# Performance work log

Hardware: AMD Instinct MI355X
Metric: run time of the kernel (lower is better)

Reference implementation:

```python
import jax, jax.numpy as jnp
from jax import lax
import numpy as np

B, H, W, D_MODEL = 2, 64, 64, 192
D_INNER, D_STATE, DT_RANK = 384, 16, 12
L = H * W
LN_EPS = 1e-5


def setup_inputs() -> dict:
    ks = jax.random.split(jax.random.key(0), 12)
    rng = np.random.default_rng(0)
    perm = rng.permutation(L).astype(np.int32)

    def p(i, shape, scale=0.02):
        return jax.random.normal(ks[i], shape, dtype=jnp.float32) * scale

    return {
        "x": jax.random.normal(ks[0], (B, H, W, D_MODEL), dtype=jnp.float32),
        "condition": jax.random.normal(ks[1], (B, H, W, D_MODEL), dtype=jnp.float32),
        "W_in": p(2, (2 * D_INNER, D_MODEL)),
        "W_con": p(3, (D_INNER, D_MODEL)),
        "conv_w": p(4, (D_INNER, 1, 3, 3)),
        "conv_b": jnp.zeros((D_INNER,), jnp.float32),
        "con_conv_w": p(5, (D_INNER, 1, 3, 3)),
        "con_conv_b": jnp.zeros((D_INNER,), jnp.float32),
        "x_proj_w": p(6, (DT_RANK + 2 * D_STATE, D_INNER)),
        "dt_proj_w": p(7, (D_INNER, DT_RANK)),
        "dt_proj_b": p(8, (D_INNER,), 0.1),
        "A_logs": jnp.tile(jnp.log(jnp.arange(1, D_STATE + 1, dtype=jnp.float32))[None, :], (D_INNER, 1)),
        "Ds": jnp.ones((D_INNER,), jnp.float32),
        "ln_w": jnp.ones((D_INNER,), jnp.float32),
        "ln_b": jnp.zeros((D_INNER,), jnp.float32),
        "W_out": p(9, (D_MODEL, D_INNER)),
        "scan_path": jnp.asarray(perm),
        "rev_scan_path": jnp.asarray(np.argsort(perm).astype(np.int32)),
    }


def _dwconv(x, w, b):
    # depthwise 3x3 conv, SAME padding; x: [B, C, H, W], w: [C, 1, 3, 3]
    y = lax.conv_general_dilated(x, w, (1, 1), "SAME",
                                 dimension_numbers=("NCHW", "OIHW", "NCHW"),
                                 feature_group_count=x.shape[1])
    return y + b[None, :, None, None]


def _selective_scan(u, delta, A, Bs, Cs, D):
    # u, delta: [B, D, L]; A: [D, N]; Bs, Cs: [B, N, L]; D: [D]
    dA = jnp.exp(jnp.einsum("bdl,dn->lbdn", delta, A))          # [L, B, D, N]
    dBu = jnp.einsum("bdl,bnl,bdl->lbdn", delta, Bs, u)          # [L, B, D, N]
    Ct = jnp.transpose(Cs, (2, 0, 1))                             # [L, B, N]
    h0 = jnp.zeros(dA.shape[1:], dA.dtype)

    def step(h, inp):
        a, b, c = inp
        h = a * h + b
        return h, jnp.einsum("bdn,bn->bd", h, c)

    _, ys = lax.scan(step, h0, (dA, dBu, Ct))                     # ys: [L, B, D]
    y = jnp.transpose(ys, (1, 2, 0))                              # [B, D, L]
    return y + u * D[None, :, None]


def _forward(x, condition, W_in, W_con, conv_w, conv_b, con_conv_w, con_conv_b,
             x_proj_w, dt_proj_w, dt_proj_b, A_logs, Ds, ln_w, ln_b, W_out,
             scan_path, rev_scan_path):
    b, h, w, _ = x.shape
    l = h * w
    xz = x @ W_in.T                                               # [B, H, W, 2*Din]
    xa, z = jnp.split(xz, 2, axis=-1)
    z = jax.nn.silu(z)
    c = condition @ W_con.T
    xa = jax.nn.silu(_dwconv(jnp.transpose(xa, (0, 3, 1, 2)), conv_w, conv_b))
    c = jax.nn.silu(_dwconv(jnp.transpose(c, (0, 3, 1, 2)), con_conv_w, con_conv_b))
    d = xa.shape[1]
    xs = xa.reshape(b, d, l)[:, :, scan_path]                     # forward_permutation, K=1
    cs = c.reshape(b, d, l)[:, :, scan_path]
    x_dbl = jnp.einsum("bdl,cd->bcl", xs + cs, x_proj_w)          # [B, R+2N, L]
    r, n = dt_proj_w.shape[1], A_logs.shape[1]
    dts = jnp.einsum("brl,dr->bdl", x_dbl[:, :r], dt_proj_w)
    Bs = x_dbl[:, r:r + n]
    Cs = x_dbl[:, r + n:]
    A = -jnp.exp(A_logs)
    delta = jax.nn.softplus(dts + dt_proj_b[None, :, None])       # delta_softplus=True
    y = _selective_scan(xs, delta, A, Bs, Cs, Ds)                 # [B, D, L]
    y = y[:, :, rev_scan_path]                                    # backward_permutation
    y = jnp.transpose(y, (0, 2, 1))                               # [B, L, D]
    mu = jnp.mean(y, axis=-1, keepdims=True)
    var = jnp.var(y, axis=-1, keepdims=True)
    y = (y - mu) * lax.rsqrt(var + LN_EPS) * ln_w + ln_b          # out_norm
    y = y.reshape(b, h, w, d) * z
    return y @ W_out.T                                            # out_proj (no bias)


def reference(x, condition, W_in, W_con, conv_w, conv_b, con_conv_w, con_conv_b,
              x_proj_w, dt_proj_w, dt_proj_b, A_logs, Ds, ln_w, ln_b, W_out,
              scan_path, rev_scan_path):
    return _forward(x, condition, W_in, W_con, conv_w, conv_b, con_conv_w,
                    con_conv_b, x_proj_w, dt_proj_w, dt_proj_b, A_logs, Ds,
                    ln_w, ln_b, W_out, scan_path, rev_scan_path)
```

## Files before the change

kernel.cpp:

```cpp
#include <hip/hip_runtime.h>
#include <math.h>

#define BB 2
#define HH 64
#define WW 64
#define DM 192
#define DI 384
#define NS 16
#define DTR 12
#define LL 4096
#define ROWS (BB*LL)
#define NCHUNK 128
#define LCHUNK 32
#define NCOMB 448
#define CSTRIDE ((size_t)BB * DI * 8)

typedef __attribute__((ext_vector_type(8))) short bf16x8;
typedef __attribute__((ext_vector_type(4))) float f32x4;

typedef __attribute__((address_space(3))) void        as3_void;
typedef __attribute__((address_space(1))) const void  as1_cvoid;

__device__ __forceinline__ void gl_lds16(const unsigned short* g, unsigned short* l) {
    __builtin_amdgcn_global_load_lds((as1_cvoid*)g, (as3_void*)l, 16, 0, 0);
}

#define WAITCNT_BARRIER(N)                                         \
    do {                                                           \
        asm volatile("s_waitcnt vmcnt(" #N ")" ::: "memory");      \
        __builtin_amdgcn_s_barrier();                              \
        asm volatile("" ::: "memory");                             \
    } while (0)

__device__ __forceinline__ float silu_f(float v) {
    return v / (1.0f + __expf(-v));
}

__device__ __forceinline__ unsigned short f2bf(float f) {
    union { float f; unsigned int u; } c; c.f = f;
    unsigned int u = c.u;
    u += 0x7fffu + ((u >> 16) & 1u);
    return (unsigned short)(u >> 16);
}
__device__ __forceinline__ float bf2f(unsigned short h) {
    union { unsigned int u; float f; } c; c.u = ((unsigned int)h) << 16;
    return c.f;
}

__global__ __launch_bounds__(256) void prep_weights(
    const float* __restrict__ x, const float* __restrict__ cond,
    const float* __restrict__ w_in, const float* __restrict__ w_con,
    const float* __restrict__ w_out,
    const float* __restrict__ x_proj_w, const float* __restrict__ dt_w,
    unsigned short* __restrict__ w_in_bf, unsigned short* __restrict__ w_con_bf,
    unsigned short* __restrict__ w_out_bf, unsigned short* __restrict__ wc,
    unsigned short* __restrict__ x_bfo, unsigned short* __restrict__ c_bfo)
{
    int idx = blockIdx.x * 256 + threadIdx.x;
    if (idx < 73728) {
        const float4* src; ushort4* dst; int off;
        if (idx < 36864)      { src = (const float4*)w_in;  dst = (ushort4*)w_in_bf;  off = idx; }
        else if (idx < 55296) { src = (const float4*)w_con; dst = (ushort4*)w_con_bf; off = idx - 36864; }
        else                  { src = (const float4*)w_out; dst = (ushort4*)w_out_bf; off = idx - 55296; }
        float4 v = src[off];
        ushort4 o;
        o.x = f2bf(v.x); o.y = f2bf(v.y); o.z = f2bf(v.z); o.w = f2bf(v.w);
        dst[off] = o;
    } else if (idx < 73728 + NCOMB * DI) {
        int e = idx - 73728;
        int row = e / DI, k = e - row * DI;
        float v = 0.f;
        if (row < 384) {
            const float* dw = dt_w + row * DTR;
            #pragma unroll
            for (int r = 0; r < DTR; ++r) v += dw[r] * x_proj_w[r * DI + k];
        } else if (row < 416) {
            v = x_proj_w[(12 + (row - 384)) * DI + k];
        }
        wc[e] = f2bf(v);
    } else if (idx < 73728 + NCOMB * DI + 786432) {
        int e = idx - (73728 + NCOMB * DI);
        const float4* src; ushort4* dst; int off;
        if (e < 393216) { src = (const float4*)x;    dst = (ushort4*)x_bfo; off = e; }
        else            { src = (const float4*)cond; dst = (ushort4*)c_bfo; off = e - 393216; }
        float4 v = src[off];
        ushort4 o;
        o.x = f2bf(v.x); o.y = f2bf(v.y); o.z = f2bf(v.z); o.w = f2bf(v.w);
        dst[off] = o;
    }
}

__global__ __launch_bounds__(256) void gemm_in(
    const unsigned short* __restrict__ x_bf, const unsigned short* __restrict__ cin_bf,
    const unsigned short* __restrict__ w_in_bf,
    const unsigned short* __restrict__ w_con_bf,
    unsigned short* __restrict__ xa_bf, unsigned short* __restrict__ z_bf,
    unsigned short* __restrict__ c_bf)
{
    const int y  = blockIdx.y;
    const int zz = (y >= 12) ? 1 : 0;
    const unsigned short* A = zz ? cin_bf : x_bf;
    const unsigned short* W = zz ? w_con_bf : w_in_bf;
    const int bn = (zz ? (y - 12) : y) * 64;
    const int bm = blockIdx.x * 64;

    __shared__ __align__(16) unsigned short sA[4 * 64 * 32];
    __shared__ __align__(16) unsigned short sB[4 * 64 * 32];
    const int tid  = threadIdx.x;
    const int wave = tid >> 6;
    const int lane = tid & 63;
    const int quad = lane >> 4;
    const int l16  = lane & 15;
    const int srow = tid >> 2;
    const int scol = ((tid & 3) ^ ((tid >> 3) & 3)) * 8;
    const int rswz = (quad ^ ((l16 >> 1) & 3)) * 8;

    f32x4 acc[4];
    #pragma unroll
    for (int t = 0; t < 4; ++t) acc[t] = (f32x4)(0.f);

    const unsigned short* gA = &A[(size_t)(bm + srow) * DM + scol];
    const unsigned short* gB = &W[(size_t)(bn + srow) * DM + scol];

    #pragma unroll
    for (int p = 0; p < 3; ++p) {
        gl_lds16(gA + p * 32, &sA[p * 2048 + wave * 512]);
        gl_lds16(gB + p * 32, &sB[p * 2048 + wave * 512]);
    }
    WAITCNT_BARRIER(4);

    const int ar = (wave * 16 + l16) * 32 + rswz;

    #pragma unroll
    for (int t = 0; t < 6; ++t) {
        if (t + 3 < 6) {
            const int k = (t + 3) * 32, pb = (t + 3) & 3;
            gl_lds16(gA + k, &sA[pb * 2048 + wave * 512]);
            gl_lds16(gB + k, &sB[pb * 2048 + wave * 512]);
        }
        const unsigned short* cA = &sA[(t & 3) * 2048];
        const unsigned short* cB = &sB[(t & 3) * 2048];
        bf16x8 a = *(bf16x8*)&cA[ar];
        #pragma unroll
        for (int n = 0; n < 4; ++n) {
            bf16x8 b = *(bf16x8*)&cB[(n * 16 + l16) * 32 + rswz];
            acc[n] = __builtin_amdgcn_mfma_f32_16x16x32_bf16(a, b, acc[n], 0, 0, 0);
        }
        if (t < 5) {
            if (t + 3 < 6)      WAITCNT_BARRIER(4);
            else if (t + 2 < 6) WAITCNT_BARRIER(2);
            else                WAITCNT_BARRIER(0);
        }
    }

    #pragma unroll
    for (int n = 0; n < 4; ++n) {
        int col = bn + n * 16 + l16;
        #pragma unroll
        for (int r = 0; r < 4; ++r) {
            int row = bm + wave * 16 + quad * 4 + r;
            float v = acc[n][r];
            if (zz == 0) {
                if (col < 384) xa_bf[(size_t)row * 384 + col] = f2bf(v);
                else           z_bf[(size_t)row * 384 + (col - 384)] = f2bf(silu_f(v));
            } else {
                c_bf[(size_t)row * 384 + col] = f2bf(v);
            }
        }
    }
}

__global__ __launch_bounds__(256) void gemm_comb(
    const unsigned short* __restrict__ A, const unsigned short* __restrict__ W,
    const float* __restrict__ bias, float* __restrict__ btct,
    unsigned short* __restrict__ du_lo)
{
    __shared__ __align__(16) unsigned short sA[4 * 64 * 32];
    __shared__ __align__(16) unsigned short sB[4 * 64 * 32];
    const int bm = blockIdx.x * 64;
    const int bn = blockIdx.y * 64;
    const int tid  = threadIdx.x;
    const int wave = tid >> 6;
    const int lane = tid & 63;
    const int quad = lane >> 4;
    const int l16  = lane & 15;
    const int srow = tid >> 2;
    const int scol = ((tid & 3) ^ ((tid >> 3) & 3)) * 8;
    const int rswz = (quad ^ ((l16 >> 1) & 3)) * 8;

    f32x4 acc[4];
    #pragma unroll
    for (int t = 0; t < 4; ++t) acc[t] = (f32x4)(0.f);

    const unsigned short* gA = &A[(size_t)(bm + srow) * DI + scol];
    const unsigned short* gB = &W[(size_t)(bn + srow) * DI + scol];

    #pragma unroll
    for (int p = 0; p < 3; ++p) {
        gl_lds16(gA + p * 32, &sA[p * 2048 + wave * 512]);
        gl_lds16(gB + p * 32, &sB[p * 2048 + wave * 512]);
    }
    WAITCNT_BARRIER(4);

    const int ar = (wave * 16 + l16) * 32 + rswz;

    #pragma unroll
    for (int t = 0; t < 12; ++t) {
        if (t + 3 < 12) {
            const int k = (t + 3) * 32, pb = (t + 3) & 3;
            gl_lds16(gA + k, &sA[pb * 2048 + wave * 512]);
            gl_lds16(gB + k, &sB[pb * 2048 + wave * 512]);
        }
        const unsigned short* cA = &sA[(t & 3) * 2048];
        const unsigned short* cB = &sB[(t & 3) * 2048];
        bf16x8 a = *(bf16x8*)&cA[ar];
        #pragma unroll
        for (int n = 0; n < 4; ++n) {
            bf16x8 b = *(bf16x8*)&cB[(n * 16 + l16) * 32 + rswz];
            acc[n] = __builtin_amdgcn_mfma_f32_16x16x32_bf16(a, b, acc[n], 0, 0, 0);
        }
        if (t < 11) {
            if (t + 3 < 12)      WAITCNT_BARRIER(4);
            else if (t + 2 < 12) WAITCNT_BARRIER(2);
            else                 WAITCNT_BARRIER(0);
        }
    }

    #pragma unroll
    for (int n = 0; n < 4; ++n) {
        int col = bn + n * 16 + l16;
        #pragma unroll
        for (int r = 0; r < 4; ++r) {
            int row = bm + wave * 16 + quad * 4 + r;
            float v = acc[n][r];
            if (col < 384) {
                float a = v + bias[col];
                float sp = (a > 20.f) ? a : log1pf(__expf(a));
                du_lo[((size_t)row * 384 + col) * 2] = f2bf(sp);
            } else if (col < 416) {
                int idx = col - 384;
                int pos = (idx < 16) ? ((idx & 7) * 4 + (idx >> 3))
                                     : (((idx - 16) & 7) * 4 + 2 + ((idx - 16) >> 3));
                btct[(size_t)row * 32 + pos] = v;
            }
        }
    }
}

__global__ __launch_bounds__(256) void gemm_out_fused(
    const unsigned short* __restrict__ yt, const unsigned short* __restrict__ z,
    const int* __restrict__ rev_path,
    const float* __restrict__ ln_w, const float* __restrict__ ln_b,
    const unsigned short* __restrict__ W, float* __restrict__ out)
{
    __shared__ __align__(16) unsigned short sA[32 * 392];
    __shared__ __align__(16) unsigned short sB[3 * 64 * 32];
    const int bm = blockIdx.x * 32;
    const int bn = blockIdx.y * 64;
    const int tid = threadIdx.x;
    const int r2  = tid >> 3;
    const int q8  = tid & 7;
    const int b   = bm >> 12;
    const int l   = (bm & (LL - 1)) + r2;
    const int js  = rev_path[l];

    const unsigned short* yrow = yt + ((size_t)(b * LL + js)) * DI;
    const unsigned short* zrow = z  + ((size_t)(b * LL + l)) * DI;

    bf16x8 yv[6];
    float s = 0.f, s2 = 0.f;
    #pragma unroll
    for (int i = 0; i < 6; ++i) {
        yv[i] = *(const bf16x8*)&yrow[i * 64 + q8 * 8];
        #pragma unroll
        for (int e = 0; e < 8; ++e) {
            float f = bf2f((unsigned short)yv[i][e]);
            s += f; s2 += f * f;
        }
    }
    s  += __shfl_xor(s, 1);  s  += __shfl_xor(s, 2);  s  += __shfl_xor(s, 4);
    s2 += __shfl_xor(s2, 1); s2 += __shfl_xor(s2, 2); s2 += __shfl_xor(s2, 4);
    const float mu  = s * (1.0f / DI);
    const float inv = rsqrtf(s2 * (1.0f / DI) - mu * mu + 1e-5f);

    #pragma unroll
    for (int i = 0; i < 6; ++i) {
        int c = i * 64 + q8 * 8;
        bf16x8 zv = *(const bf16x8*)&zrow[c];
        float4 wa = *(const float4*)&ln_w[c];
        float4 wb = *(const float4*)&ln_w[c + 4];
        float4 ba = *(const float4*)&ln_b[c];
        float4 bb = *(const float4*)&ln_b[c + 4];
        bf16x8 o;
        o[0] = (short)f2bf(((bf2f((unsigned short)yv[i][0]) - mu) * inv * wa.x + ba.x) * bf2f((unsigned short)zv[0]));
        o[1] = (short)f2bf(((bf2f((unsigned short)yv[i][1]) - mu) * inv * wa.y + ba.y) * bf2f((unsigned short)zv[1]));
        o[2] = (short)f2bf(((bf2f((unsigned short)yv[i][2]) - mu) * inv * wa.z + ba.z) * bf2f((unsigned short)zv[2]));
        o[3] = (short)f2bf(((bf2f((unsigned short)yv[i][3]) - mu) * inv * wa.w + ba.w) * bf2f((unsigned short)zv[3]));
        o[4] = (short)f2bf(((bf2f((unsigned short)yv[i][4]) - mu) * inv * wb.x + bb.x) * bf2f((unsigned short)zv[4]));
        o[5] = (short)f2bf(((bf2f((unsigned short)yv[i][5]) - mu) * inv * wb.y + bb.y) * bf2f((unsigned short)zv[5]));
        o[6] = (short)f2bf(((bf2f((unsigned short)yv[i][6]) - mu) * inv * wb.z + bb.z) * bf2f((unsigned short)zv[6]));
        o[7] = (short)f2bf(((bf2f((unsigned short)yv[i][7]) - mu) * inv * wb.w + bb.w) * bf2f((unsigned short)zv[7]));
        *(bf16x8*)&sA[r2 * 392 + c] = o;
    }

    const int wave = tid >> 6;
    const int lane = tid & 63;
    const int quad = lane >> 4;
    const int l16  = lane & 15;
    const int srow = tid >> 2;
    const int scol = ((tid & 3) ^ ((tid >> 3) & 3)) * 8;
    const int rswz = (quad ^ ((l16 >> 1) & 3)) * 8;
    const int rf   = wave >> 1;
    const int np   = (wave & 1) * 2;

    f32x4 acc[2];
    acc[0] = (f32x4)(0.f); acc[1] = (f32x4)(0.f);

    const unsigned short* gB = &W[(size_t)(bn + srow) * DI + scol];
    const int abase = (rf * 16 + l16) * 392 + quad * 8;

    gl_lds16(gB,      &sB[0 * 2048 + wave * 512]);
    gl_lds16(gB + 32, &sB[1 * 2048 + wave * 512]);
    __syncthreads();

    #pragma unroll
    for (int t = 0; t < 12; ++t) {
        if (t + 2 < 12)
            gl_lds16(gB + (t + 2) * 32, &sB[((t + 2) % 3) * 2048 + wave * 512]);
        bf16x8 a = *(bf16x8*)&sA[abase + t * 32];
        const unsigned short* cB = &sB[(t % 3) * 2048];
        #pragma unroll
        for (int k = 0; k < 2; ++k) {
            bf16x8 bfr = *(bf16x8*)&cB[((np + k) * 16 + l16) * 32 + rswz];
            acc[k] = __builtin_amdgcn_mfma_f32_16x16x32_bf16(a, bfr, acc[k], 0, 0, 0);
        }
        if (t < 11) {
            if (t + 2 < 12) WAITCNT_BARRIER(1);
            else            WAITCNT_BARRIER(0);
        }
    }

    #pragma unroll
    for (int k = 0; k < 2; ++k) {
        int col = bn + (np + k) * 16 + l16;
        #pragma unroll
        for (int rr = 0; rr < 4; ++rr) {
            int row = bm + rf * 16 + quad * 4 + rr;
            out[(size_t)row * DM + col] = acc[k][rr];
        }
    }
}

__global__ __launch_bounds__(256) void dwconv2_scatter(
    const unsigned short* __restrict__ xin, const unsigned short* __restrict__ cin,
    const float* __restrict__ wx, const float* __restrict__ bx,
    const float* __restrict__ wc, const float* __restrict__ bc,
    const int* __restrict__ rev_scan_path,
    unsigned short* __restrict__ du_hi,
    unsigned short* __restrict__ s_bf)
{
    const int tile = blockIdx.x;
    const int c0   = blockIdx.y * 32;
    const int b    = blockIdx.z;
    const int h0 = (tile >> 3) * 8, w0 = (tile & 7) * 8;
    __shared__ float smx[10 * 10 * 32];
    __shared__ float smc[10 * 10 * 32];
    __shared__ int   jtile[64];

    for (int idx = threadIdx.x; idx < 800; idx += 256) {
        int pix = idx >> 3, cq = (idx & 7) * 4;
        int py = pix / 10, px = pix - py * 10;
        int gh = h0 + py - 1, gw = w0 + px - 1;
        float4 fx = make_float4(0.f, 0.f, 0.f, 0.f);
        float4 fc = make_float4(0.f, 0.f, 0.f, 0.f);
        if (gh >= 0 && gh < 64 && gw >= 0 && gw < 64) {
            size_t g = ((size_t)(b * LL + gh * 64 + gw)) * DI + c0 + cq;
            ushort4 vx = *(const ushort4*)&xin[g];
            ushort4 vc = *(const ushort4*)&cin[g];
            fx = make_float4(bf2f(vx.x), bf2f(vx.y), bf2f(vx.z), bf2f(vx.w));
            fc = make_float4(bf2f(vc.x), bf2f(vc.y), bf2f(vc.z), bf2f(vc.w));
        }
        *(float4*)&smx[pix * 32 + cq] = fx;
        *(float4*)&smc[pix * 32 + cq] = fc;
    }
    if (threadIdx.x < 64) {
        int l = (h0 + (threadIdx.x >> 3)) * 64 + (w0 + (threadIdx.x & 7));
        jtile[threadIdx.x] = rev_scan_path[l];
    }
    __syncthreads();

    const int ch = threadIdx.x & 31;
    const int pq = threadIdx.x >> 5;
    float wrx[9], wrc[9];
    #pragma unroll
    for (int k = 0; k < 9; ++k) {
        wrx[k] = wx[(c0 + ch) * 9 + k];
        wrc[k] = wc[(c0 + ch) * 9 + k];
    }
    const float bvx = bx[c0 + ch];
    const float bvc = bc[c0 + ch];

    #pragma unroll
    for (int i = 0; i < 8; ++i) {
        int p  = pq * 8 + i;
        int ph = p >> 3, pw = p & 7;
        float ax = bvx, ac = bvc;
        #pragma unroll
        for (int ki = 0; ki < 3; ++ki)
            #pragma unroll
            for (int kj = 0; kj < 3; ++kj) {
                int si = ((ph + ki) * 10 + (pw + kj)) * 32 + ch;
                ax += wrx[ki * 3 + kj] * smx[si];
                ac += wrc[ki * 3 + kj] * smc[si];
            }
        float xv = silu_f(ax);
        float sv = xv + silu_f(ac);
        size_t o = ((size_t)(b * LL + jtile[p])) * DI + c0 + ch;
        du_hi[o * 2 + 1] = f2bf(xv);
        s_bf[o]          = f2bf(sv);
    }
}

__global__ __launch_bounds__(256) void scan_chunkA(
    const unsigned int* __restrict__ du, const float* __restrict__ btct,
    const float* __restrict__ A_logs,
    float* __restrict__ chunkA, float* __restrict__ chunkB)
{
    const int c = blockIdx.x;
    const int g = blockIdx.y;
    const int b = blockIdx.z;
    const int t = threadIdx.x;
    const int grp = t >> 3, p = t & 7;
    const int d = g * 32 + grp;
    const float Av0 = -__expf(A_logs[d * NS + p]);
    const float Av1 = -__expf(A_logs[d * NS + p + 8]);
    const int j0 = c * LCHUNK;

    const unsigned int* dul = du + ((size_t)b * LL + j0) * DI + d;
    const float2*       bl  = (const float2*)btct + ((size_t)b * LL + j0) * 16 + p * 2;

    float h0 = 0.f, h1 = 0.f, Sd = 0.f;
    unsigned int duv[4]; float2 bv[4];
    #pragma unroll
    for (int q = 0; q < 4; ++q) {
        duv[q] = dul[(size_t)q * DI]; bv[q] = bl[(size_t)q * 16];
    }
    for (int j = 0; j < LCHUNK; j += 4) {
        unsigned int ndu[4]; float2 nb[4];
        if (j + 4 < LCHUNK) {
            #pragma unroll
            for (int q = 0; q < 4; ++q) {
                int jj = j + 4 + q;
                ndu[q] = dul[(size_t)jj * DI]; nb[q] = bl[(size_t)jj * 16];
            }
        }
        #pragma unroll
        for (int q = 0; q < 4; ++q) {
            float dv = bf2f((unsigned short)(duv[q] & 0xffff));
            float uv = bf2f((unsigned short)(duv[q] >> 16));
            float e0 = __expf(dv * Av0);
            float e1 = __expf(dv * Av1);
            float duu = dv * uv;
            h0 = e0 * h0 + bv[q].x * duu;
            h1 = e1 * h1 + bv[q].y * duu;
            Sd += dv;
        }
        #pragma unroll
        for (int q = 0; q < 4; ++q) { duv[q]=ndu[q]; bv[q]=nb[q]; }
    }
    size_t idx = (size_t)c * CSTRIDE + ((size_t)b * DI + d) * 8 + p;
    ((float2*)chunkA)[idx] = make_float2(__expf(Sd * Av0), __expf(Sd * Av1));
    ((float2*)chunkB)[idx] = make_float2(h0, h1);
}

__global__ __launch_bounds__(256) void scan_chunkC(
    const unsigned int* __restrict__ du, const float* __restrict__ btct,
    const float* __restrict__ A_logs, const float* __restrict__ Ds,
    const float* __restrict__ chunkA, const float* __restrict__ chunkB,
    unsigned short* __restrict__ yt)
{
    const int c = blockIdx.x;
    const int g = blockIdx.y;
    const int b = blockIdx.z;
    const int t = threadIdx.x;
    const int grp = t >> 3, p = t & 7;
    const int d = g * 32 + grp;
    const float Av0 = -__expf(A_logs[d * NS + p]);
    const float Av1 = -__expf(A_logs[d * NS + p + 8]);
    const float Dv = Ds[d];
    const int j0 = c * LCHUNK;

    const unsigned int* dul = du + ((size_t)b * LL + j0) * DI + d;
    const float4*       bcl = (const float4*)btct + ((size_t)b * LL + j0) * 8 + p;
    unsigned short* yl = yt + ((size_t)b * LL + j0) * DI + d;

    const size_t off = ((size_t)b * DI + d) * 8 + p;
    const float2* A2 = (const float2*)chunkA;
    const float2* B2 = (const float2*)chunkB;
    float h0 = 0.f, h1 = 0.f, P0 = 1.f, P1 = 1.f;
    for (int i = c - 1; i >= 0; --i) {
        size_t ix = (size_t)i * CSTRIDE + off;
        float2 a = A2[ix], bv = B2[ix];
        h0 += P0 * bv.x;  h1 += P1 * bv.y;
        P0 *= a.x;        P1 *= a.y;
        if (fmaxf(fabsf(P0), fabsf(P1)) < 1e-30f) break;
    }

    unsigned int duv[4]; float4 bc[4];
    #pragma unroll
    for (int q = 0; q < 4; ++q) {
        duv[q] = dul[(size_t)q * DI]; bc[q] = bcl[(size_t)q * 8];
    }
    for (int j = 0; j < LCHUNK; j += 4) {
        unsigned int ndu[4]; float4 nbc[4];
        if (j + 4 < LCHUNK) {
            #pragma unroll
            for (int q = 0; q < 4; ++q) {
                int jj = j + 4 + q;
                ndu[q] = dul[(size_t)jj * DI]; nbc[q] = bcl[(size_t)jj * 8];
            }
        }
        #pragma unroll
        for (int q = 0; q < 4; ++q) {
            float dv = bf2f((unsigned short)(duv[q] & 0xffff));
            float uv = bf2f((unsigned short)(duv[q] >> 16));
            float e0 = __expf(dv * Av0);
            float e1 = __expf(dv * Av1);
            float duu = dv * uv;
            h0 = e0 * h0 + bc[q].x * duu;
            h1 = e1 * h1 + bc[q].y * duu;
            float acc = h0 * bc[q].z + h1 * bc[q].w;
            acc += __shfl_xor(acc, 4, 8);
            acc += __shfl_xor(acc, 2, 8);
            acc += __shfl_xor(acc, 1, 8);
            if (p == 0) yl[(size_t)(j + q) * DI] = f2bf(acc + uv * Dv);
        }
        #pragma unroll
        for (int q = 0; q < 4; ++q) { duv[q]=ndu[q]; bc[q]=nbc[q]; }
    }
}

extern "C" void kernel_launch(void* const* d_in, const int* in_sizes, int n_in,
                              void* d_out, int out_size, void* d_ws, size_t ws_size,
                              hipStream_t stream) {
    const float* x          = (const float*)d_in[0];
    const float* cond       = (const float*)d_in[1];
    const float* W_in       = (const float*)d_in[2];
    const float* W_con      = (const float*)d_in[3];
    const float* conv_w     = (const float*)d_in[4];
    const float* conv_b     = (const float*)d_in[5];
    const float* con_conv_w = (const float*)d_in[6];
    const float* con_conv_b = (const float*)d_in[7];
    const float* x_proj_w   = (const float*)d_in[8];
    const float* dt_proj_w  = (const float*)d_in[9];
    const float* dt_proj_b  = (const float*)d_in[10];
    const float* A_logs     = (const float*)d_in[11];
    const float* Ds         = (const float*)d_in[12];
    const float* ln_w       = (const float*)d_in[13];
    const float* ln_b       = (const float*)d_in[14];
    const float* W_out      = (const float*)d_in[15];
    const int*   scan_path  = (const int*)d_in[16];
    const int*   rev_path   = (const int*)d_in[17];
    (void)scan_path;

    float* ws = (float*)d_ws;
    const size_t S  = (size_t)BB * LL * DI;
    const size_t SC = (size_t)NCHUNK * BB * DI * NS;
    float* ytslab  = ws + 0 * S;
    float* zslab   = ws + 1 * S;
    float* duslab  = ws + 2 * S;
    float* btct    = ws + 3 * S;
    float* chunkA  = btct + (size_t)BB * LL * 32;
    float* chunkB  = chunkA + SC;
    float* bfpool  = chunkB + SC;

    unsigned short* yt_bf    = (unsigned short*)ytslab;
    unsigned short* z_bf     = (unsigned short*)zslab;
    unsigned int*   du       = (unsigned int*)duslab;
    unsigned short* s_bf     = (unsigned short*)bfpool;
    unsigned short* xa_bf    = s_bf + (size_t)ROWS * DI;
    unsigned short* c_bf     = xa_bf + (size_t)ROWS * DI;
    unsigned short* w_in_bf  = c_bf + (size_t)ROWS * DI;
    unsigned short* w_con_bf = w_in_bf + 768 * DM;
    unsigned short* w_out_bf = w_con_bf + 384 * DM;
    unsigned short* wcomb_bf = w_out_bf + 192 * DI;
    unsigned short* x_bf2    = wcomb_bf + (size_t)NCOMB * DI;
    unsigned short* cin_bf2  = x_bf2 + (size_t)ROWS * DM;

    prep_weights<<<4032, 256, 0, stream>>>(
        x, cond, W_in, W_con, W_out, x_proj_w, dt_proj_w,
        w_in_bf, w_con_bf, w_out_bf, wcomb_bf, x_bf2, cin_bf2);

    gemm_in<<<dim3(ROWS / 64, 18), 256, 0, stream>>>(
        x_bf2, cin_bf2, w_in_bf, w_con_bf, xa_bf, z_bf, c_bf);
    dwconv2_scatter<<<dim3(64, 12, BB), 256, 0, stream>>>(
        xa_bf, c_bf, conv_w, conv_b, con_conv_w, con_conv_b,
        rev_path, (unsigned short*)du, s_bf);
    gemm_comb<<<dim3(ROWS / 64, NCOMB / 64), 256, 0, stream>>>(
        s_bf, wcomb_bf, dt_proj_b, btct, (unsigned short*)du);
    scan_chunkA<<<dim3(NCHUNK, DI / 32, BB), 256, 0, stream>>>(
        du, btct, A_logs, chunkA, chunkB);
    scan_chunkC<<<dim3(NCHUNK, DI / 32, BB), 256, 0, stream>>>(
        du, btct, A_logs, Ds, chunkA, chunkB, yt_bf);
    gemm_out_fused<<<dim3(ROWS / 32, DM / 64), 256, 0, stream>>>(
        yt_bf, z_bf, rev_path, ln_w, ln_b, w_out_bf, (float*)d_out);
}
```

Baseline: 197.4 us.

## Fuse bf16 conversion of inputs and weights into gemm_in, drop prep kernel

Removes the separate prep_weights kernel. gemm_in now loads fp32 activations and weights directly, converts them to bf16 in registers and stores them to a double-buffered LDS tile with register prefetch, replacing the async global-to-LDS path. An extra grid row of blocks builds the combined dt/x_proj weight and converts W_out. This saves one launch and a full bf16 round trip for x and condition through global memory. In exchange each weight tile is re-read and re-converted in fp32 by every block, global loads are synchronous, and the extra blocks of gemm_in are only one row deep.

```diff
diff --git a/kernel.cpp b/kernel.cpp
--- a/kernel.cpp
+++ b/kernel.cpp
@@ -47,109 +47,103 @@
     return c.f;
 }
 
-__global__ __launch_bounds__(256) void prep_weights(
+__device__ __forceinline__ bf16x8 f2bf8(float4 a, float4 b) {
+    bf16x8 r;
+    r[0] = (short)f2bf(a.x); r[1] = (short)f2bf(a.y);
+    r[2] = (short)f2bf(a.z); r[3] = (short)f2bf(a.w);
+    r[4] = (short)f2bf(b.x); r[5] = (short)f2bf(b.y);
+    r[6] = (short)f2bf(b.z); r[7] = (short)f2bf(b.w);
+    return r;
+}
+
+__global__ __launch_bounds__(256) void gemm_in(
     const float* __restrict__ x, const float* __restrict__ cond,
     const float* __restrict__ w_in, const float* __restrict__ w_con,
+    const float* __restrict__ x_proj_w, const float* __restrict__ dt_w,
     const float* __restrict__ w_out,
-    const float* __restrict__ x_proj_w, const float* __restrict__ dt_w,
-    unsigned short* __restrict__ w_in_bf, unsigned short* __restrict__ w_con_bf,
-    unsigned short* __restrict__ w_out_bf, unsigned short* __restrict__ wc,
-    unsigned short* __restrict__ x_bfo, unsigned short* __restrict__ c_bfo)
+    unsigned short* __restrict__ xa_bf, unsigned short* __restrict__ z_bf,
+    unsigned short* __restrict__ c_bf,
+    unsigned short* __restrict__ wcomb_bf, unsigned short* __restrict__ w_out_bf)
 {
-    int idx = blockIdx.x * 256 + threadIdx.x;
-    if (idx < 73728) {
-        const float4* src; ushort4* dst; int off;
-        if (idx < 36864)      { src = (const float4*)w_in;  dst = (ushort4*)w_in_bf;  off = idx; }
-        else if (idx < 55296) { src = (const float4*)w_con; dst = (ushort4*)w_con_bf; off = idx - 36864; }
-        else                  { src = (const float4*)w_out; dst = (ushort4*)w_out_bf; off = idx - 55296; }
-        float4 v = src[off];
-        ushort4 o;
-        o.x = f2bf(v.x); o.y = f2bf(v.y); o.z = f2bf(v.z); o.w = f2bf(v.w);
-        dst[off] = o;
-    } else if (idx < 73728 + NCOMB * DI) {
-        int e = idx - 73728;
-        int row = e / DI, k = e - row * DI;
-        float v = 0.f;
-        if (row < 384) {
-            const float* dw = dt_w + row * DTR;
-            #pragma unroll
-            for (int r = 0; r < DTR; ++r) v += dw[r] * x_proj_w[r * DI + k];
-        } else if (row < 416) {
-            v = x_proj_w[(12 + (row - 384)) * DI + k];
-        }
-        wc[e] = f2bf(v);
-    } else if (idx < 73728 + NCOMB * DI + 786432) {
-        int e = idx - (73728 + NCOMB * DI);
-        const float4* src; ushort4* dst; int off;
-        if (e < 393216) { src = (const float4*)x;    dst = (ushort4*)x_bfo; off = e; }
-        else            { src = (const float4*)cond; dst = (ushort4*)c_bfo; off = e - 393216; }
-        float4 v = src[off];
-        ushort4 o;
-        o.x = f2bf(v.x); o.y = f2bf(v.y); o.z = f2bf(v.z); o.w = f2bf(v.w);
-        dst[off] = o;
-    }
-}
-
-__global__ __launch_bounds__(256) void gemm_in(
-    const unsigned short* __restrict__ x_bf, const unsigned short* __restrict__ cin_bf,
-    const unsigned short* __restrict__ w_in_bf,
-    const unsigned short* __restrict__ w_con_bf,
-    unsigned short* __restrict__ xa_bf, unsigned short* __restrict__ z_bf,
-    unsigned short* __restrict__ c_bf)
-{
-    const int y  = blockIdx.y;
+    const int y = blockIdx.y;
+    __shared__ __align__(16) unsigned short sA[2 * 64 * 32];
+    __shared__ __align__(16) unsigned short sB[2 * 64 * 32];
+
+    if (y == 18) {
+        const int base = blockIdx.x * 256 + threadIdx.x;
+        for (int i = base; i < 18432; i += 32768) {
+            float4 v = ((const float4*)w_out)[i];
+            ushort4 o;
+            o.x = f2bf(v.x); o.y = f2bf(v.y); o.z = f2bf(v.z); o.w = f2bf(v.w);
+            ((ushort4*)w_out_bf)[i] = o;
+        }
+        for (int e = base; e < NCOMB * DI; e += 32768) {
+            int row = e / DI, k = e - row * DI;
+            float v = 0.f;
+            if (row < 384) {
+                const float* dw = dt_w + row * DTR;
+                #pragma unroll
+                for (int r = 0; r < DTR; ++r) v += dw[r] * x_proj_w[r * DI + k];
+            } else if (row < 416) {
+                v = x_proj_w[(12 + (row - 384)) * DI + k];
+            }
+            wcomb_bf[e] = f2bf(v);
+        }
+        return;
+    }
+
     const int zz = (y >= 12) ? 1 : 0;
-    const unsigned short* A = zz ? cin_bf : x_bf;
-    const unsigned short* W = zz ? w_con_bf : w_in_bf;
+    const float* A = zz ? cond : x;
+    const float* W = zz ? w_con : w_in;
     const int bn = (zz ? (y - 12) : y) * 64;
     const int bm = blockIdx.x * 64;
 
-    __shared__ __align__(16) unsigned short sA[4 * 64 * 32];
-    __shared__ __align__(16) unsigned short sB[4 * 64 * 32];
     const int tid  = threadIdx.x;
     const int wave = tid >> 6;
     const int lane = tid & 63;
     const int quad = lane >> 4;
     const int l16  = lane & 15;
     const int srow = tid >> 2;
-    const int scol = ((tid & 3) ^ ((tid >> 3) & 3)) * 8;
+    const int q4   = tid & 3;
+    const int wcol = (q4 ^ ((srow >> 1) & 3)) * 8;
     const int rswz = (quad ^ ((l16 >> 1) & 3)) * 8;
 
     f32x4 acc[4];
     #pragma unroll
     for (int t = 0; t < 4; ++t) acc[t] = (f32x4)(0.f);
 
-    const unsigned short* gA = &A[(size_t)(bm + srow) * DM + scol];
-    const unsigned short* gB = &W[(size_t)(bn + srow) * DM + scol];
-
-    #pragma unroll
-    for (int p = 0; p < 3; ++p) {
-        gl_lds16(gA + p * 32, &sA[p * 2048 + wave * 512]);
-        gl_lds16(gB + p * 32, &sB[p * 2048 + wave * 512]);
-    }
-    WAITCNT_BARRIER(4);
+    const float* gA = &A[(size_t)(bm + srow) * DM + q4 * 8];
+    const float* gB = &W[(size_t)(bn + srow) * DM + q4 * 8];
+
+    float4 ra0 = *(const float4*)gA,        ra1 = *(const float4*)(gA + 4);
+    float4 rb0 = *(const float4*)gB,        rb1 = *(const float4*)(gB + 4);
+    *(bf16x8*)&sA[srow * 32 + wcol] = f2bf8(ra0, ra1);
+    *(bf16x8*)&sB[srow * 32 + wcol] = f2bf8(rb0, rb1);
+    ra0 = *(const float4*)(gA + 32); ra1 = *(const float4*)(gA + 36);
+    rb0 = *(const float4*)(gB + 32); rb1 = *(const float4*)(gB + 36);
 
     const int ar = (wave * 16 + l16) * 32 + rswz;
 
     #pragma unroll
     for (int t = 0; t < 6; ++t) {
-        if (t + 3 < 6) {
-            const int k = (t + 3) * 32, pb = (t + 3) & 3;
-            gl_lds16(gA + k, &sA[pb * 2048 + wave * 512]);
-            gl_lds16(gB + k, &sB[pb * 2048 + wave * 512]);
-        }
-        const unsigned short* cA = &sA[(t & 3) * 2048];
-        const unsigned short* cB = &sB[(t & 3) * 2048];
+        __syncthreads();
+        const unsigned short* cA = &sA[(t & 1) * 2048];
+        const unsigned short* cB = &sB[(t & 1) * 2048];
         bf16x8 a = *(bf16x8*)&cA[ar];
+        if (t + 1 < 6) {
+            const int nb = (t + 1) & 1;
+            *(bf16x8*)&sA[nb * 2048 + srow * 32 + wcol] = f2bf8(ra0, ra1);
+            *(bf16x8*)&sB[nb * 2048 + srow * 32 + wcol] = f2bf8(rb0, rb1);
+            if (t + 2 < 6) {
+                const int k = (t + 2) * 32;
+                ra0 = *(const float4*)(gA + k); ra1 = *(const float4*)(gA + k + 4);
+                rb0 = *(const float4*)(gB + k); rb1 = *(const float4*)(gB + k + 4);
+            }
+        }
         #pragma unroll
         for (int n = 0; n < 4; ++n) {
             bf16x8 b = *(bf16x8*)&cB[(n * 16 + l16) * 32 + rswz];
             acc[n] = __builtin_amdgcn_mfma_f32_16x16x32_bf16(a, b, acc[n], 0, 0, 0);
-        }
-        if (t < 5) {
-            if (t + 3 < 6)      WAITCNT_BARRIER(4);
-            else if (t + 2 < 6) WAITCNT_BARRIER(2);
-            else                WAITCNT_BARRIER(0);
         }
     }
 
@@ -580,19 +574,12 @@
     unsigned short* s_bf     = (unsigned short*)bfpool;
     unsigned short* xa_bf    = s_bf + (size_t)ROWS * DI;
     unsigned short* c_bf     = xa_bf + (size_t)ROWS * DI;
-    unsigned short* w_in_bf  = c_bf + (size_t)ROWS * DI;
-    unsigned short* w_con_bf = w_in_bf + 768 * DM;
-    unsigned short* w_out_bf = w_con_bf + 384 * DM;
+    unsigned short* w_out_bf = c_bf + (size_t)ROWS * DI;
     unsigned short* wcomb_bf = w_out_bf + 192 * DI;
-    unsigned short* x_bf2    = wcomb_bf + (size_t)NCOMB * DI;
-    unsigned short* cin_bf2  = x_bf2 + (size_t)ROWS * DM;
-
-    prep_weights<<<4032, 256, 0, stream>>>(
-        x, cond, W_in, W_con, W_out, x_proj_w, dt_proj_w,
-        w_in_bf, w_con_bf, w_out_bf, wcomb_bf, x_bf2, cin_bf2);
-
-    gemm_in<<<dim3(ROWS / 64, 18), 256, 0, stream>>>(
-        x_bf2, cin_bf2, w_in_bf, w_con_bf, xa_bf, z_bf, c_bf);
+
+    gemm_in<<<dim3(ROWS / 64, 19), 256, 0, stream>>>(
+        x, cond, W_in, W_con, x_proj_w, dt_proj_w, W_out,
+        xa_bf, z_bf, c_bf, wcomb_bf, w_out_bf);
     dwconv2_scatter<<<dim3(64, 12, BB), 256, 0, stream>>>(
         xa_bf, c_bf, conv_w, conv_b, con_conv_w, con_conv_b,
         rev_path, (unsigned short*)du, s_bf);
```

Measured after the change: 196.9 us (median of 2 runs). No clear change (-0.2%).
